# Performance work log

Measured on AMD Instinct MI355X. Metric: run time of the kernel, lower is better.

The kernel has to match this reference:

```python
import jax, jax.numpy as jnp
import numpy as np

B, L, D, H = 2, 2048, 1024, 16
HD = D // H  # 64


def rotate_half(x):
    x1, x2 = x[..., : x.shape[-1] // 2], x[..., x.shape[-1] // 2 :]
    return jnp.concatenate([-x2, x1], axis=-1)


def apply_rope(x, cos, sin):
    # x: (B, H, L, HD); cos/sin: (1, L, HD)
    c = cos[:, None, : x.shape[2], :]
    s = sin[:, None, : x.shape[2], :]
    return x * c + rotate_half(x) * s


def setup_inputs() -> dict:
    key = jax.random.key(0)
    ks = jax.random.split(key, 16)
    query = jax.random.normal(ks[0], (B, L, D), jnp.float32)
    k_in = jax.random.normal(ks[1], (B, L, D), jnp.float32)
    v_in = jax.random.normal(ks[2], (B, L, D), jnp.float32)
    key_padding_mask = jax.random.uniform(ks[3], (B, L)) < 0.2
    # genuine RoPE tables
    inv_freq = 1.0 / (10000.0 ** (jnp.arange(0, HD, 2, dtype=jnp.float32) / HD))
    ang = jnp.arange(L, dtype=jnp.float32)[:, None] * inv_freq[None, :]  # (L, HD/2)
    ang = jnp.concatenate([ang, ang], axis=-1)  # (L, HD)
    rope_cos = jnp.cos(ang)[None]  # (1, L, HD)
    rope_sin = jnp.sin(ang)[None]
    scale = 0.02
    Wq = jax.random.normal(ks[4], (D, D), jnp.float32) * scale
    bq = jnp.zeros((D,), jnp.float32)
    Wk = jax.random.normal(ks[5], (D, D), jnp.float32) * scale
    bk = jnp.zeros((D,), jnp.float32)
    Wv = jax.random.normal(ks[6], (D, D), jnp.float32) * scale
    bv = jnp.zeros((D,), jnp.float32)
    Wg = jax.random.normal(ks[7], (D, D), jnp.float32) * scale  # init zeros in torch; random for grad coverage
    bg = jnp.ones((D,), jnp.float32)
    Wo = jax.random.normal(ks[8], (D, D), jnp.float32) * scale
    bo = jnp.zeros((D,), jnp.float32)
    return dict(query=query, key=k_in, value=v_in, key_padding_mask=key_padding_mask,
                rope_cos=rope_cos, rope_sin=rope_sin,
                Wq=Wq, bq=bq, Wk=Wk, bk=bk, Wv=Wv, bv=bv,
                Wg=Wg, bg=bg, Wo=Wo, bo=bo)


def reference(query, key, value, key_padding_mask, rope_cos, rope_sin,
              Wq, bq, Wk, bk, Wv, bv, Wg, bg, Wo, bo):
    Bq, Lq, _ = query.shape
    Lk = key.shape[1]
    # torch Linear: x @ W.T + b
    Q = (query @ Wq.T + bq).reshape(Bq, Lq, H, HD).transpose(0, 2, 1, 3)
    K = (key @ Wk.T + bk).reshape(Bq, Lk, H, HD).transpose(0, 2, 1, 3)
    V = (value @ Wv.T + bv).reshape(Bq, Lk, H, HD).transpose(0, 2, 1, 3)
    K = apply_rope(K, rope_cos, rope_sin)
    Q = apply_rope(Q, rope_cos, rope_sin)
    scale = 1.0 / jnp.sqrt(jnp.asarray(HD, query.dtype))
    scores = jnp.einsum('bhqd,bhkd->bhqk', Q, K) * scale
    allow = ~key_padding_mask[:, None, None, :]  # (B,1,1,Lk): True = attend
    scores = jnp.where(allow, scores, -jnp.inf)
    attn = jax.nn.softmax(scores, axis=-1)
    out = jnp.einsum('bhqk,bhkd->bhqd', attn, V)
    out = jnp.nan_to_num(out, nan=0.0)
    out = out.transpose(0, 2, 1, 3).reshape(Bq, Lq, D)
    gate = jax.nn.sigmoid(query @ Wg.T + bg)
    out = out * gate
    out = out @ Wo.T + bo
    return out
```

## Files before the change

kernel.cpp:

```cpp
#include <hip/hip_runtime.h>
#include <hip/hip_bf16.h>
#include <cstdint>


constexpr int NB = 2, NL = 2048, ND = 1024, NH = 16, NHD = 64;
constexpr int NM = NB * NL;

typedef __bf16 bf16_t;
typedef __bf16 bf16x8 __attribute__((ext_vector_type(8)));
typedef __bf16 bf16x4 __attribute__((ext_vector_type(4)));
typedef float f32x4 __attribute__((ext_vector_type(4)));
typedef float f32x16 __attribute__((ext_vector_type(16)));
typedef unsigned int uint2v __attribute__((ext_vector_type(2)));

typedef const __attribute__((address_space(1))) void* gas_ptr;
typedef __attribute__((address_space(3))) void* las_ptr;

__device__ __forceinline__ void async_load16(const void* g, void* l) {
  __builtin_amdgcn_global_load_lds((gas_ptr)g, (las_ptr)l, 16, 0, 0);
}

__device__ __forceinline__ unsigned cvtpk_bf16(float lo, float hi) {
  unsigned r;
  asm("v_cvt_pk_bf16_f32 %0, %1, %2" : "=v"(r) : "v"(lo), "v"(hi));
  return r;
}

__device__ __forceinline__ void pl32_swap(unsigned& a, unsigned& b) {
#if __has_builtin(__builtin_amdgcn_permlane32_swap)
  uint2v r = __builtin_amdgcn_permlane32_swap(a, b, false, false);
  a = r.x; b = r.y;
#else
  asm volatile("v_permlane32_swap_b32 %0, %1" : "+v"(a), "+v"(b));
#endif
}

__device__ __forceinline__ float fast_exp2(float x) {
#if __has_builtin(__builtin_amdgcn_exp2f)
  return __builtin_amdgcn_exp2f(x);
#else
  float r;
  asm("v_exp_f32 %0, %1" : "=v"(r) : "v"(x));
  return r;
#endif
}

struct CvtArgs {
  const float* s[8];
  bf16_t* d[8];
};
__global__ __launch_bounds__(256) void cvt8_kernel(CvtArgs a) {
  int y = blockIdx.y;
  int n4 = (y < 3) ? (NM * ND / 4) : (ND * ND / 4);
  const float* src = a.s[y];
  bf16_t* dst = a.d[y];
  for (int i = blockIdx.x * 256 + threadIdx.x; i < n4; i += gridDim.x * 256) {
    float4 v = ((const float4*)src)[i];
    bf16x4 o;
    o[0] = (bf16_t)v.x; o[1] = (bf16_t)v.y; o[2] = (bf16_t)v.z; o[3] = (bf16_t)v.w;
    ((bf16x4*)dst)[i] = o;
  }
}

__global__ __launch_bounds__(512, 2) void gemm8_kernel(
    const bf16_t* __restrict__ Aq, const bf16_t* __restrict__ Ak, const bf16_t* __restrict__ Av,
    const bf16_t* __restrict__ W0, const bf16_t* __restrict__ W1,
    const bf16_t* __restrict__ W2, const bf16_t* __restrict__ W3,
    const float* __restrict__ b0, const float* __restrict__ b1,
    const float* __restrict__ b2, const float* __restrict__ b3,
    const float* __restrict__ ctab, const float* __restrict__ stab,
    bf16_t* __restrict__ Qr, bf16_t* __restrict__ Kr, bf16_t* __restrict__ Vt,
    bf16_t* __restrict__ Gb) {
  extern __shared__ __align__(16) bf16_t smem[];
  bf16_t* lA = smem;
  bf16_t* lB = smem + 32768;

  const int tid = threadIdx.x, lane = tid & 63, w = tid >> 6;
  const int wm = w >> 2, wn = w & 3;
  const int lr = lane & 15, lg = lane >> 4;

  const int lin = blockIdx.x;
  const int xcd = lin & 7, idx = lin >> 3;
  const int nt = xcd * 2 + (idx & 1);
  const int mt = idx >> 1;
  const int t = nt >> 2;
  const bf16_t* Asrc = (t == 1) ? Ak : (t == 2) ? Av : Aq;
  const bf16_t* Wsrc = (t == 0) ? W0 : (t == 1) ? W1 : (t == 2) ? W2 : W3;
  const int nbase = (nt & 3) * 256;

  const int srow = lane >> 3;
  const int gcol = ((lane & 7) ^ srow) * 8;

  auto stageA = [&](int buf, int hf, int kt) {
#pragma unroll
    for (int jj = 0; jj < 2; ++jj) {
      int slot = jj * 8 + w;
      int r = slot * 8 + srow;
      async_load16(Asrc + (size_t)(mt * 256 + hf * 128 + r) * ND + kt * 64 + gcol,
                   lA + (buf * 2 + hf) * 8192 + slot * 512);
    }
  };
  auto stageB = [&](int buf, int hf, int kt) {
#pragma unroll
    for (int jj = 0; jj < 2; ++jj) {
      int slot = jj * 8 + w;
      int r = slot * 8 + srow;
      async_load16(Wsrc + (size_t)(nbase + hf * 128 + r) * ND + kt * 64 + gcol,
                   lB + (buf * 2 + hf) * 8192 + slot * 512);
    }
  };

  f32x4 acc[8][4];
#pragma unroll
  for (int i = 0; i < 8; ++i)
#pragma unroll
    for (int j = 0; j < 4; ++j)
#pragma unroll
      for (int k = 0; k < 4; ++k) acc[i][j][k] = 0.f;

  stageA(0, 0, 0); stageA(0, 1, 0); stageB(0, 0, 0); stageB(0, 1, 0);
  stageB(1, 0, 1); stageB(1, 1, 1);
  asm volatile("s_waitcnt vmcnt(4)" ::: "memory");
  __builtin_amdgcn_s_barrier();

  const bf16_t* Ab[2] = { lA + wm * 8192, lA + (2 + wm) * 8192 };
  const bf16_t* Bb[2] = { lB + (wn >> 1) * 8192 + (wn & 1) * 4096,
                          lB + (2 + (wn >> 1)) * 8192 + (wn & 1) * 4096 };

  for (int j = 0; j < 8; ++j) {
#pragma unroll
    for (int hp = 0; hp < 2; ++hp) {
      const bf16_t* Ap = Ab[hp];
      const bf16_t* Bp = Bb[hp];
      bf16x8 bfr[4][2];
#pragma unroll
      for (int p = 0; p < 4; ++p) {
        bf16x8 af[2][2];
#pragma unroll
        for (int mi = 0; mi < 2; ++mi)
#pragma unroll
          for (int ks = 0; ks < 2; ++ks)
            af[mi][ks] = *(const bf16x8*)(Ap + ((p * 2 + mi) * 16 + lr) * 64 +
                                          ((ks * 4 + lg) ^ (lr & 7)) * 8);
        if (p == 0) {
#pragma unroll
          for (int nj = 0; nj < 4; ++nj)
#pragma unroll
            for (int ks = 0; ks < 2; ++ks)
              bfr[nj][ks] = *(const bf16x8*)(Bp + (nj * 16 + lr) * 64 +
                                             ((ks * 4 + lg) ^ (lr & 7)) * 8);
        }
        if (hp == 0) {
          if (p == 0) stageA(1, 0, 2 * j + 1);
          if (p == 1) { stageA(1, 1, 2 * j + 1); if (j < 7) stageB(0, 0, 2 * j + 2); }
          if (p == 2) { if (j < 7) stageB(0, 1, 2 * j + 2); }
        } else if (j < 7) {
          if (p == 0) stageA(0, 0, 2 * j + 2);
          if (p == 1) { stageA(0, 1, 2 * j + 2); stageB(1, 0, 2 * j + 3); }
          if (p == 2) stageB(1, 1, 2 * j + 3);
        }
        __builtin_amdgcn_s_barrier();
        __builtin_amdgcn_s_setprio(1);
#pragma unroll
        for (int mi = 0; mi < 2; ++mi)
#pragma unroll
          for (int nj = 0; nj < 4; ++nj)
#pragma unroll
            for (int ks = 0; ks < 2; ++ks)
              acc[p * 2 + mi][nj] = __builtin_amdgcn_mfma_f32_16x16x32_bf16(
                  af[mi][ks], bfr[nj][ks], acc[p * 2 + mi][nj], 0, 0, 0);
        __builtin_amdgcn_s_setprio(0);
        if (p == 3) {
          if (hp == 0) {
            if (j < 7) { asm volatile("s_waitcnt vmcnt(4)" ::: "memory"); }
            else       { asm volatile("s_waitcnt vmcnt(0)" ::: "memory"); }
          } else if (j < 7) {
            asm volatile("s_waitcnt vmcnt(4)" ::: "memory");
          }
        }
        __builtin_amdgcn_s_barrier();
      }
    }
  }

  const int fbase = nbase + wn * 64;
  const int h = fbase >> 6;
  if (t < 2) {
    bf16_t* dst = (t == 0) ? Qr : Kr;
    const float* bias = (t == 0) ? b0 : b1;
    const float qs = (t == 0) ? 0.18033688011112042f : 1.0f;
#pragma unroll
    for (int i = 0; i < 8; ++i)
#pragma unroll
      for (int rg = 0; rg < 4; ++rg) {
        int mm = mt * 256 + wm * 128 + i * 16 + lg * 4 + rg;
        int bb = mm >> 11, l = mm & (NL - 1);
        bf16_t* rowp = dst + ((bb * NH + h) * NL + l) * NHD;
        const float* crow = ctab + l * NHD;
        const float* srw = stab + l * NHD;
#pragma unroll
        for (int nj = 0; nj < 2; ++nj) {
          int dlo = nj * 16 + lr, dhi = dlo + 32;
          float xlo = acc[i][nj][rg] + bias[fbase + dlo];
          float xhi = acc[i][nj + 2][rg] + bias[fbase + dhi];
          float olo = (xlo * crow[dlo] - xhi * srw[dlo]) * qs;
          float ohi = (xhi * crow[dhi] + xlo * srw[dhi]) * qs;
          rowp[dlo] = (bf16_t)olo;
          rowp[dhi] = (bf16_t)ohi;
        }
      }
  } else if (t == 2) {
#pragma unroll
    for (int i = 0; i < 8; ++i) {
      int mmb = mt * 256 + wm * 128 + i * 16 + lg * 4;
      int bb = mmb >> 11, l0 = mmb & (NL - 1);
#pragma unroll
      for (int nj = 0; nj < 4; ++nj) {
        int d = nj * 16 + lr;
        float bias = b2[fbase + d];
        unsigned u01 = cvtpk_bf16(acc[i][nj][0] + bias, acc[i][nj][1] + bias);
        unsigned u23 = cvtpk_bf16(acc[i][nj][2] + bias, acc[i][nj][3] + bias);
        unsigned long long pk = (unsigned long long)u01 | ((unsigned long long)u23 << 32);
        *(unsigned long long*)(Vt + ((bb * NH + h) * NHD + d) * NL + l0) = pk;
      }
    }
  } else {
#pragma unroll
    for (int i = 0; i < 8; ++i)
#pragma unroll
      for (int rg = 0; rg < 4; ++rg) {
        int mm = mt * 256 + wm * 128 + i * 16 + lg * 4 + rg;
#pragma unroll
        for (int nj = 0; nj < 4; ++nj) {
          int f = fbase + nj * 16 + lr;
          Gb[mm * ND + f] = (bf16_t)(acc[i][nj][rg] + b3[f]);
        }
      }
  }
}

__global__ __launch_bounds__(256) void gemm_out_kernel(
    const bf16_t* __restrict__ A, const bf16_t* __restrict__ W,
    const float* __restrict__ bias0, float* __restrict__ Out) {
  __shared__ __align__(16) bf16_t lA[2][128 * 64];
  __shared__ __align__(16) bf16_t lB[2][128 * 64];
  const int tid = threadIdx.x, lane = tid & 63, w = tid >> 6;
  const int wm = w >> 1, wn = w & 1;
  const int lr = lane & 15, lg = lane >> 4;

  const int lin = blockIdx.x;
  const int ntile = lin & 7, mtile = lin >> 3;

  const bf16_t* Ablk = A + mtile * 128 * ND;
  const bf16_t* Wblk = W + ntile * 128 * ND;

  f32x4 acc[4][4];
#pragma unroll
  for (int i = 0; i < 4; ++i)
#pragma unroll
    for (int j = 0; j < 4; ++j)
#pragma unroll
      for (int k = 0; k < 4; ++k) acc[i][j][k] = 0.f;

  auto STAGE = [&](int b, int kb) {
#pragma unroll
    for (int p = 0; p < 4; ++p) {
      int q = w * 256 + p * 64 + lane;
      int r = q >> 3, c = q & 7;
      int cs = c ^ (r & 7);
      async_load16(Ablk + r * ND + kb * 64 + cs * 8, &lA[b][(w * 256 + p * 64) * 8]);
      async_load16(Wblk + r * ND + kb * 64 + cs * 8, &lB[b][(w * 256 + p * 64) * 8]);
    }
  };
  auto COMPUTE = [&](int b) {
    const bf16_t* pA = lA[b];
    const bf16_t* pB = lB[b];
#pragma unroll
    for (int ks = 0; ks < 2; ++ks) {
      bf16x8 af[4], bfr[4];
#pragma unroll
      for (int i = 0; i < 4; ++i) {
        int ra = wm * 64 + i * 16 + lr;
        int ca = (ks * 4 + lg) ^ (ra & 7);
        af[i] = *(const bf16x8*)(pA + ra * 64 + ca * 8);
        int rb = wn * 64 + i * 16 + lr;
        int cb = (ks * 4 + lg) ^ (rb & 7);
        bfr[i] = *(const bf16x8*)(pB + rb * 64 + cb * 8);
      }
#pragma unroll
      for (int i = 0; i < 4; ++i)
#pragma unroll
        for (int j = 0; j < 4; ++j)
          acc[i][j] = __builtin_amdgcn_mfma_f32_16x16x32_bf16(af[i], bfr[j], acc[i][j], 0, 0, 0);
    }
  };

  STAGE(0, 0);
  __syncthreads();
  int buf = 0;
  for (int kb = 0; kb < 15; ++kb) {
    STAGE(buf ^ 1, kb + 1);
    COMPUTE(buf);
    __syncthreads();
    buf ^= 1;
  }
  COMPUTE(buf);

#pragma unroll
  for (int j = 0; j < 4; ++j) {
    int nn = ntile * 128 + wn * 64 + j * 16 + lr;
    float bias = bias0[nn];
#pragma unroll
    for (int i = 0; i < 4; ++i)
#pragma unroll
      for (int rg = 0; rg < 4; ++rg) {
        int mm = mtile * 128 + wm * 64 + i * 16 + lg * 4 + rg;
        Out[mm * ND + nn] = acc[i][j][rg] + bias;
      }
  }
}

__global__ __launch_bounds__(256) void attn_kernel(
    const bf16_t* __restrict__ Qr, const bf16_t* __restrict__ Kr, const bf16_t* __restrict__ Vt,
    const int* __restrict__ mask, const bf16_t* __restrict__ Gb, bf16_t* __restrict__ X) {
  __shared__ __align__(16) bf16_t lK[2][128 * 64];
  __shared__ __align__(16) bf16_t lV[2][64 * 128];

  int lin = blockIdx.y * gridDim.x + blockIdx.x;
  int swz = (lin & 7) * 64 + (lin >> 3);
  const int qb = swz & 15, bh = swz >> 4;
  const int bb = bh >> 4, h = bh & 15;

  const int tid = threadIdx.x, lane = tid & 63, w = tid >> 6;
  const int ql = lane & 31, hi = lane >> 5;

  const bf16_t* Kbh = Kr + bh * NL * NHD;
  const bf16_t* Vbh = Vt + bh * NHD * NL;
  const int q = qb * 128 + w * 32 + ql;

  const bf16_t* Qp = Qr + (bh * NL + q) * NHD + 8 * hi;
  bf16x8 qf[4];
#pragma unroll
  for (int c = 0; c < 4; ++c) qf[c] = *(const bf16x8*)(Qp + 16 * c);
  bf16x8 qf5 = {};
  qf5[0] = (bf16_t)(hi ? 0.f : 1.f);

  f32x16 zero16;
#pragma unroll
  for (int r = 0; r < 16; ++r) zero16[r] = 0.f;
  bf16x8 ones8;
#pragma unroll
  for (int r = 0; r < 8; ++r) ones8[r] = (bf16_t)1.f;

  f32x16 acc[2];
#pragma unroll
  for (int dt = 0; dt < 2; ++dt)
#pragma unroll
    for (int r = 0; r < 16; ++r) acc[dt][r] = 0.f;
  f32x16 lacc16 = zero16;

  const bf16_t* gsrc[8];
#pragma unroll
  for (int j = 0; j < 8; ++j) {
    if (j < 4) {
      int u = j * 256 + tid;
      int r = u >> 3, c = u & 7, cs = c ^ (r & 7);
      gsrc[j] = Kbh + r * NHD + cs * 8;
    } else {
      int v = (j - 4) * 256 + tid;
      int r = v >> 4, c = v & 15, cs = (c & 8) | ((c & 7) ^ (r & 7));
      gsrc[j] = Vbh + r * NL + cs * 8;
    }
  }
  auto STAGE = [&](int b) {
#pragma unroll
    for (int j = 0; j < 8; ++j) {
      if (j < 4) {
        async_load16(gsrc[j], &lK[b][(j * 256 + tid) * 8]);
        gsrc[j] += 128 * NHD;
      } else {
        async_load16(gsrc[j], &lV[b][((j - 4) * 256 + tid) * 8]);
        gsrc[j] += 128;
      }
    }
  };

  unsigned rdK[2][4], rdV[2][4];
#pragma unroll
  for (int t2 = 0; t2 < 2; ++t2)
#pragma unroll
    for (int c = 0; c < 4; ++c) {
      unsigned un = ((2 * c + hi) ^ (ql & 7)) * 16;
      rdK[t2][c] = (32 * t2 + ql) * 128 + un;
      rdV[t2][c] = (32 * t2 + ql) * 256 + un;
    }
  const char* lKc = (const char*)lK;
  const char* lVc = (const char*)lV;

  STAGE(0);
  int mv0 = mask[bb * NL + lane];
  int mv1 = mask[bb * NL + 64 + lane];
  __syncthreads();

  auto BODY = [&](int buf, int t) {
    int nmv0 = 0, nmv1 = 0;
    if (t < 15) {
      STAGE(buf ^ 1);
      nmv0 = mask[bb * NL + (t + 1) * 128 + lane];
      nmv1 = mask[bb * NL + (t + 1) * 128 + 64 + lane];
    }
    unsigned long long bmA = __ballot(mv0 != 0);
    unsigned long long bmB = __ballot(mv1 != 0);
    unsigned mws[4] = {(unsigned)bmA, (unsigned)(bmA >> 32),
                       (unsigned)bmB, (unsigned)(bmB >> 32)};
    bf16x8 kf5[4];
#pragma unroll
    for (int g = 0; g < 4; ++g) {
      float bv = ((mws[g] >> ql) & 1u) ? -1008.f : -8.f;
      bf16x8 z = {};
      z[0] = (bf16_t)(hi ? 0.f : bv);
      kf5[g] = z;
    }
#pragma unroll
    for (int hh = 0; hh < 2; ++hh) {
      f32x16 st[2];
      __builtin_amdgcn_s_setprio(1);
#pragma unroll
      for (int t2 = 0; t2 < 2; ++t2) {
        f32x16 s = __builtin_amdgcn_mfma_f32_32x32x16_bf16(kf5[hh * 2 + t2], qf5,
                                                           zero16, 0, 0, 0);
#pragma unroll
        for (int c = 0; c < 4; ++c) {
          bf16x8 kf = *(const bf16x8*)(lKc + rdK[t2][c] + buf * 16384 + hh * 8192);
          s = __builtin_amdgcn_mfma_f32_32x32x16_bf16(kf, qf[c], s, 0, 0, 0);
        }
        st[t2] = s;
      }
      __builtin_amdgcn_s_setprio(0);

#pragma unroll
      for (int t2 = 0; t2 < 2; ++t2)
#pragma unroll
        for (int r = 0; r < 16; ++r) st[t2][r] = fast_exp2(st[t2][r]);

      unsigned wds[2][4][2];
#pragma unroll
      for (int t2 = 0; t2 < 2; ++t2)
#pragma unroll
        for (int r1 = 0; r1 < 4; ++r1) {
          wds[t2][r1][0] = cvtpk_bf16(st[t2][4 * r1 + 0], st[t2][4 * r1 + 1]);
          wds[t2][r1][1] = cvtpk_bf16(st[t2][4 * r1 + 2], st[t2][4 * r1 + 3]);
        }
      bf16x8 pf[4];
#pragma unroll
      for (int kc = 0; kc < 4; ++kc) {
        int t2 = kc >> 1, r1a = 2 * (kc & 1);
        unsigned a0 = wds[t2][r1a][0], b0 = wds[t2][r1a + 1][0];
        unsigned a1 = wds[t2][r1a][1], b1 = wds[t2][r1a + 1][1];
        pl32_swap(a0, b0);
        pl32_swap(a1, b1);
        union { unsigned u[4]; bf16x8 v; } uu;
        uu.u[0] = a0; uu.u[1] = a1; uu.u[2] = b0; uu.u[3] = b1;
        pf[kc] = uu.v;
      }

      __builtin_amdgcn_s_setprio(1);
#pragma unroll
      for (int dt = 0; dt < 2; ++dt) {
        f32x16 a = acc[dt];
#pragma unroll
        for (int kc = 0; kc < 4; ++kc) {
          bf16x8 vf = *(const bf16x8*)(lVc + rdV[dt][kc] + buf * 16384 + hh * 128);
          a = __builtin_amdgcn_mfma_f32_32x32x16_bf16(vf, pf[kc], a, 0, 0, 0);
        }
        acc[dt] = a;
      }
#pragma unroll
      for (int kc = 0; kc < 4; ++kc)
        lacc16 = __builtin_amdgcn_mfma_f32_32x32x16_bf16(ones8, pf[kc], lacc16, 0, 0, 0);
      __builtin_amdgcn_s_setprio(0);
    }
    __syncthreads();
    mv0 = nmv0;
    mv1 = nmv1;
  };

  for (int tt = 0; tt < 8; ++tt) {
    BODY(0, 2 * tt);
    BODY(1, 2 * tt + 1);
  }

  float lt = lacc16[0];
  float rinv = lt > 0.f ? 1.f / lt : 0.f;
  const int rowbase = (bb * NL + q) * ND + h * NHD;
#pragma unroll
  for (int dt = 0; dt < 2; ++dt)
#pragma unroll
    for (int r1 = 0; r1 < 4; ++r1) {
      int dbase = 32 * dt + 8 * r1 + 4 * hi;
      bf16x4 g4 = *(const bf16x4*)(Gb + rowbase + dbase);
      bf16x4 o;
#pragma unroll
      for (int j = 0; j < 4; ++j) {
        float gate = 1.f / (1.f + fast_exp2(-1.44269504f * (float)g4[j]));
        o[j] = (bf16_t)(acc[dt][4 * r1 + j] * rinv * gate);
      }
      *(bf16x4*)(X + rowbase + dbase) = o;
    }
}

extern "C" void kernel_launch(void* const* d_in, const int* in_sizes, int n_in,
                              void* d_out, int out_size, void* d_ws, size_t ws_size,
                              hipStream_t stream) {
  const float* query = (const float*)d_in[0];
  const float* key   = (const float*)d_in[1];
  const float* value = (const float*)d_in[2];
  const int*   maskp = (const int*)d_in[3];
  const float* rcos  = (const float*)d_in[4];
  const float* rsin  = (const float*)d_in[5];
  const float* Wq = (const float*)d_in[6];  const float* bq = (const float*)d_in[7];
  const float* Wk = (const float*)d_in[8];  const float* bk = (const float*)d_in[9];
  const float* Wv = (const float*)d_in[10]; const float* bv = (const float*)d_in[11];
  const float* Wg = (const float*)d_in[12]; const float* bg = (const float*)d_in[13];
  const float* Wo = (const float*)d_in[14]; const float* bo = (const float*)d_in[15];

  constexpr size_t MB = 1ull << 20;
  char* ws = (char*)d_ws;
  bf16_t* qbb = (bf16_t*)(ws + 0 * MB);
  bf16_t* kbb = (bf16_t*)(ws + 8 * MB);
  bf16_t* vbb = (bf16_t*)(ws + 16 * MB);
  bf16_t* wqb = (bf16_t*)(ws + 24 * MB);
  bf16_t* wkb = (bf16_t*)(ws + 26 * MB);
  bf16_t* wvb = (bf16_t*)(ws + 28 * MB);
  bf16_t* wgb = (bf16_t*)(ws + 30 * MB);
  bf16_t* wob = (bf16_t*)(ws + 32 * MB);
  bf16_t* Qr  = (bf16_t*)(ws + 34 * MB);
  bf16_t* Kr  = (bf16_t*)(ws + 42 * MB);
  bf16_t* Vt  = (bf16_t*)(ws + 50 * MB);
  bf16_t* Gb  = (bf16_t*)(ws + 58 * MB);
  bf16_t* Xb  = (bf16_t*)(ws + 74 * MB);

  CvtArgs ca;
  ca.s[0] = query; ca.d[0] = qbb;
  ca.s[1] = key;   ca.d[1] = kbb;
  ca.s[2] = value; ca.d[2] = vbb;
  ca.s[3] = Wq;    ca.d[3] = wqb;
  ca.s[4] = Wk;    ca.d[4] = wkb;
  ca.s[5] = Wv;    ca.d[5] = wvb;
  ca.s[6] = Wg;    ca.d[6] = wgb;
  ca.s[7] = Wo;    ca.d[7] = wob;
  cvt8_kernel<<<dim3(1024, 8), 256, 0, stream>>>(ca);

  gemm8_kernel<<<256, 512, 131072, stream>>>(
      qbb, kbb, vbb, wqb, wkb, wvb, wgb, bq, bk, bv, bg, rcos, rsin,
      Qr, Kr, Vt, Gb);

  attn_kernel<<<dim3(16, 32), 256, 0, stream>>>(Qr, Kr, Vt, maskp, Gb, Xb);

  gemm_out_kernel<<<256, 256, 0, stream>>>(Xb, wob, bo, (float*)d_out);
}
```

Measured before the change: 132.3 us.

## Pipeline attention K/V loads with 4-slot ring of 64-key tiles and precomputed mask

Replaces the double-buffered 128-key K/V staging with a 4-slot ring of 64-key tiles, prefetched three tiles ahead. It synchronises with vmcnt waits plus a single barrier per tile instead of a full __syncthreads. The key padding mask is ballot-packed once into shared memory up front, which removes the per-tile global mask loads and ballots. The goal is deeper memory latency hiding, at the cost of more barriers (32 tiles instead of 16) and hand-counted vmcnt values, which are fragile.

```diff
diff --git a/kernel.cpp b/kernel.cpp
--- a/kernel.cpp
+++ b/kernel.cpp
@@ -323,8 +323,8 @@
 __global__ __launch_bounds__(256) void attn_kernel(
     const bf16_t* __restrict__ Qr, const bf16_t* __restrict__ Kr, const bf16_t* __restrict__ Vt,
     const int* __restrict__ mask, const bf16_t* __restrict__ Gb, bf16_t* __restrict__ X) {
-  __shared__ __align__(16) bf16_t lK[2][128 * 64];
-  __shared__ __align__(16) bf16_t lV[2][64 * 128];
+  __shared__ __align__(16) bf16_t lKV[4][8192];
+  __shared__ unsigned long long lMaskQ[32];
 
   int lin = blockIdx.y * gridDim.x + blockIdx.x;
   int swz = (lin & 7) * 64 + (lin >> 3);
@@ -359,29 +359,22 @@
     for (int r = 0; r < 16; ++r) acc[dt][r] = 0.f;
   f32x16 lacc16 = zero16;
 
-  const bf16_t* gsrc[8];
-#pragma unroll
-  for (int j = 0; j < 8; ++j) {
-    if (j < 4) {
-      int u = j * 256 + tid;
-      int r = u >> 3, c = u & 7, cs = c ^ (r & 7);
-      gsrc[j] = Kbh + r * NHD + cs * 8;
-    } else {
-      int v = (j - 4) * 256 + tid;
-      int r = v >> 4, c = v & 15, cs = (c & 8) | ((c & 7) ^ (r & 7));
-      gsrc[j] = Vbh + r * NL + cs * 8;
-    }
-  }
-  auto STAGE = [&](int b) {
-#pragma unroll
-    for (int j = 0; j < 8; ++j) {
-      if (j < 4) {
-        async_load16(gsrc[j], &lK[b][(j * 256 + tid) * 8]);
-        gsrc[j] += 128 * NHD;
-      } else {
-        async_load16(gsrc[j], &lV[b][((j - 4) * 256 + tid) * 8]);
-        gsrc[j] += 128;
-      }
+  const bf16_t* gK[2];
+  const bf16_t* gV[2];
+#pragma unroll
+  for (int j = 0; j < 2; ++j) {
+    int u = j * 256 + tid;
+    int r = u >> 3, c = u & 7, cs = c ^ (r & 7);
+    gK[j] = Kbh + r * NHD + cs * 8;
+    gV[j] = Vbh + r * NL + cs * 8;
+  }
+  auto STAGE = [&](int slot) {
+#pragma unroll
+    for (int j = 0; j < 2; ++j) {
+      async_load16(gK[j], &lKV[slot][(j * 256 + tid) * 8]);
+      gK[j] += 64 * NHD;
+      async_load16(gV[j], &lKV[slot][4096 + (j * 256 + tid) * 8]);
+      gV[j] += 64;
     }
   };
 
@@ -392,103 +385,94 @@
     for (int c = 0; c < 4; ++c) {
       unsigned un = ((2 * c + hi) ^ (ql & 7)) * 16;
       rdK[t2][c] = (32 * t2 + ql) * 128 + un;
-      rdV[t2][c] = (32 * t2 + ql) * 256 + un;
-    }
-  const char* lKc = (const char*)lK;
-  const char* lVc = (const char*)lV;
-
-  STAGE(0);
-  int mv0 = mask[bb * NL + lane];
-  int mv1 = mask[bb * NL + 64 + lane];
+      rdV[t2][c] = 8192 + (32 * t2 + ql) * 128 + un;
+    }
+  const char* lbase = (const char*)lKV;
+
+#pragma unroll
+  for (int j = 0; j < 8; ++j) {
+    int mv = mask[bb * NL + j * 256 + w * 64 + lane];
+    unsigned long long bmv = __ballot(mv != 0);
+    if (lane == 0) lMaskQ[j * 4 + w] = bmv;
+  }
+  STAGE(0); STAGE(1); STAGE(2);
   __syncthreads();
 
-  auto BODY = [&](int buf, int t) {
-    int nmv0 = 0, nmv1 = 0;
-    if (t < 15) {
-      STAGE(buf ^ 1);
-      nmv0 = mask[bb * NL + (t + 1) * 128 + lane];
-      nmv1 = mask[bb * NL + (t + 1) * 128 + 64 + lane];
-    }
-    unsigned long long bmA = __ballot(mv0 != 0);
-    unsigned long long bmB = __ballot(mv1 != 0);
-    unsigned mws[4] = {(unsigned)bmA, (unsigned)(bmA >> 32),
-                       (unsigned)bmB, (unsigned)(bmB >> 32)};
-    bf16x8 kf5[4];
-#pragma unroll
-    for (int g = 0; g < 4; ++g) {
-      float bv = ((mws[g] >> ql) & 1u) ? -1008.f : -8.f;
-      bf16x8 z = {};
-      z[0] = (bf16_t)(hi ? 0.f : bv);
-      kf5[g] = z;
-    }
-#pragma unroll
-    for (int hh = 0; hh < 2; ++hh) {
-      f32x16 st[2];
-      __builtin_amdgcn_s_setprio(1);
-#pragma unroll
-      for (int t2 = 0; t2 < 2; ++t2) {
-        f32x16 s = __builtin_amdgcn_mfma_f32_32x32x16_bf16(kf5[hh * 2 + t2], qf5,
-                                                           zero16, 0, 0, 0);
-#pragma unroll
-        for (int c = 0; c < 4; ++c) {
-          bf16x8 kf = *(const bf16x8*)(lKc + rdK[t2][c] + buf * 16384 + hh * 8192);
-          s = __builtin_amdgcn_mfma_f32_32x32x16_bf16(kf, qf[c], s, 0, 0, 0);
-        }
-        st[t2] = s;
-      }
-      __builtin_amdgcn_s_setprio(0);
-
-#pragma unroll
-      for (int t2 = 0; t2 < 2; ++t2)
-#pragma unroll
-        for (int r = 0; r < 16; ++r) st[t2][r] = fast_exp2(st[t2][r]);
-
-      unsigned wds[2][4][2];
-#pragma unroll
-      for (int t2 = 0; t2 < 2; ++t2)
-#pragma unroll
-        for (int r1 = 0; r1 < 4; ++r1) {
-          wds[t2][r1][0] = cvtpk_bf16(st[t2][4 * r1 + 0], st[t2][4 * r1 + 1]);
-          wds[t2][r1][1] = cvtpk_bf16(st[t2][4 * r1 + 2], st[t2][4 * r1 + 3]);
-        }
-      bf16x8 pf[4];
+  auto COMPUTE = [&](int slot, int t) {
+    unsigned long long bm = lMaskQ[t];
+    unsigned mw[2] = {(unsigned)bm, (unsigned)(bm >> 32)};
+    const char* base = lbase + slot * 16384;
+    f32x16 st[2];
+    __builtin_amdgcn_s_setprio(1);
+#pragma unroll
+    for (int t2 = 0; t2 < 2; ++t2) {
+      bf16x8 k5 = {};
+      k5[0] = (bf16_t)(hi ? 0.f : (((mw[t2] >> ql) & 1u) ? -1008.f : -8.f));
+      f32x16 s = __builtin_amdgcn_mfma_f32_32x32x16_bf16(k5, qf5, zero16, 0, 0, 0);
+#pragma unroll
+      for (int c = 0; c < 4; ++c) {
+        bf16x8 kf = *(const bf16x8*)(base + rdK[t2][c]);
+        s = __builtin_amdgcn_mfma_f32_32x32x16_bf16(kf, qf[c], s, 0, 0, 0);
+      }
+      st[t2] = s;
+    }
+    __builtin_amdgcn_s_setprio(0);
+#pragma unroll
+    for (int t2 = 0; t2 < 2; ++t2)
+#pragma unroll
+      for (int r = 0; r < 16; ++r) st[t2][r] = fast_exp2(st[t2][r]);
+    unsigned wds[2][4][2];
+#pragma unroll
+    for (int t2 = 0; t2 < 2; ++t2)
+#pragma unroll
+      for (int r1 = 0; r1 < 4; ++r1) {
+        wds[t2][r1][0] = cvtpk_bf16(st[t2][4 * r1 + 0], st[t2][4 * r1 + 1]);
+        wds[t2][r1][1] = cvtpk_bf16(st[t2][4 * r1 + 2], st[t2][4 * r1 + 3]);
+      }
+    bf16x8 pf[4];
+#pragma unroll
+    for (int kc = 0; kc < 4; ++kc) {
+      int t2 = kc >> 1, r1a = 2 * (kc & 1);
+      unsigned a0 = wds[t2][r1a][0], b0 = wds[t2][r1a + 1][0];
+      unsigned a1 = wds[t2][r1a][1], b1 = wds[t2][r1a + 1][1];
+      pl32_swap(a0, b0);
+      pl32_swap(a1, b1);
+      union { unsigned u[4]; bf16x8 v; } uu;
+      uu.u[0] = a0; uu.u[1] = a1; uu.u[2] = b0; uu.u[3] = b1;
+      pf[kc] = uu.v;
+    }
+    __builtin_amdgcn_s_setprio(1);
+#pragma unroll
+    for (int dt = 0; dt < 2; ++dt) {
+      f32x16 a = acc[dt];
 #pragma unroll
       for (int kc = 0; kc < 4; ++kc) {
-        int t2 = kc >> 1, r1a = 2 * (kc & 1);
-        unsigned a0 = wds[t2][r1a][0], b0 = wds[t2][r1a + 1][0];
-        unsigned a1 = wds[t2][r1a][1], b1 = wds[t2][r1a + 1][1];
-        pl32_swap(a0, b0);
-        pl32_swap(a1, b1);
-        union { unsigned u[4]; bf16x8 v; } uu;
-        uu.u[0] = a0; uu.u[1] = a1; uu.u[2] = b0; uu.u[3] = b1;
-        pf[kc] = uu.v;
-      }
-
-      __builtin_amdgcn_s_setprio(1);
-#pragma unroll
-      for (int dt = 0; dt < 2; ++dt) {
-        f32x16 a = acc[dt];
-#pragma unroll
-        for (int kc = 0; kc < 4; ++kc) {
-          bf16x8 vf = *(const bf16x8*)(lVc + rdV[dt][kc] + buf * 16384 + hh * 128);
-          a = __builtin_amdgcn_mfma_f32_32x32x16_bf16(vf, pf[kc], a, 0, 0, 0);
-        }
-        acc[dt] = a;
-      }
-#pragma unroll
-      for (int kc = 0; kc < 4; ++kc)
-        lacc16 = __builtin_amdgcn_mfma_f32_32x32x16_bf16(ones8, pf[kc], lacc16, 0, 0, 0);
-      __builtin_amdgcn_s_setprio(0);
-    }
-    __syncthreads();
-    mv0 = nmv0;
-    mv1 = nmv1;
+        bf16x8 vf = *(const bf16x8*)(base + rdV[dt][kc]);
+        a = __builtin_amdgcn_mfma_f32_32x32x16_bf16(vf, pf[kc], a, 0, 0, 0);
+      }
+      acc[dt] = a;
+    }
+#pragma unroll
+    for (int kc = 0; kc < 4; ++kc)
+      lacc16 = __builtin_amdgcn_mfma_f32_32x32x16_bf16(ones8, pf[kc], lacc16, 0, 0, 0);
+    __builtin_amdgcn_s_setprio(0);
   };
 
-  for (int tt = 0; tt < 8; ++tt) {
-    BODY(0, 2 * tt);
-    BODY(1, 2 * tt + 1);
-  }
+  for (int t = 0; t < 30; ++t) {
+    asm volatile("s_waitcnt vmcnt(8)" ::: "memory");
+    __builtin_amdgcn_s_barrier();
+    __builtin_amdgcn_sched_barrier(0);
+    if (t < 29) STAGE((t + 3) & 3);
+    COMPUTE(t & 3, t);
+  }
+  asm volatile("s_waitcnt vmcnt(4)" ::: "memory");
+  __builtin_amdgcn_s_barrier();
+  __builtin_amdgcn_sched_barrier(0);
+  COMPUTE(2, 30);
+  asm volatile("s_waitcnt vmcnt(0)" ::: "memory");
+  __builtin_amdgcn_s_barrier();
+  __builtin_amdgcn_sched_barrier(0);
+  COMPUTE(3, 31);
 
   float lt = lacc16[0];
   float rinv = lt > 0.f ? 1.f / lt : 0.f;
```

Measured after the change: 135.8 us. 2.6% more time.
